# Kernel optimization log

Measured on AMD Instinct MI355X. Metric: run time of the kernel, lower is better.

## Reference

```python
import jax, jax.numpy as jnp
import numpy as np

H = 8           # num_heads
TANH_CLIP = 10.0


def setup_inputs() -> dict:
    key = jax.random.key(0)
    ks = jax.random.split(key, 7)
    B, N, D = 512, 1000, 128
    embeddings = jax.random.normal(ks[0], (B, N, D), dtype=jnp.float32)
    context_feat = jax.random.normal(ks[1], (B, 2 * D), dtype=jnp.float32)
    W_node = jax.random.normal(ks[2], (D, 3 * D), dtype=jnp.float32) / np.sqrt(D)
    W_fixed = jax.random.normal(ks[3], (D, D), dtype=jnp.float32) / np.sqrt(D)
    W_step = jax.random.normal(ks[4], (2 * D, D), dtype=jnp.float32) / np.sqrt(2 * D)
    W_out = jax.random.normal(ks[5], (D, D), dtype=jnp.float32) / np.sqrt(D)
    # action_mask: True = feasible node; ensure at least one feasible per row
    action_mask = jax.random.uniform(ks[6], (B, N)) > 0.3
    action_mask = action_mask.at[:, 0].set(True)
    return {"embeddings": embeddings, "context_feat": context_feat,
            "W_node": W_node, "W_fixed": W_fixed, "W_step": W_step,
            "W_out": W_out, "action_mask": action_mask}


def reference(embeddings, context_feat, W_node, W_fixed, W_step, W_out, action_mask):
    B, N, D = embeddings.shape
    dk = D // H
    # --- _precompute ---
    graph_context = (embeddings.mean(axis=1) @ W_fixed)[:, None, :]      # [B,1,D]
    proj = embeddings @ W_node                                            # [B,N,3D]
    gk, gv, logit_k = jnp.split(proj, 3, axis=-1)                         # each [B,N,D]
    to_heads = lambda x: x.reshape(B, N, H, dk).transpose(2, 0, 1, 3)     # [H,B,N,dk]
    K, V = to_heads(gk), to_heads(gv)
    # --- _get_log_p: query (num_steps = 1) ---
    q = graph_context + (context_feat @ W_step)[:, None, :]               # [B,1,D]
    Q = q.reshape(B, 1, H, dk).transpose(2, 0, 1, 3)                      # [H,B,1,dk]
    mask = ~action_mask                                                    # [B,N], True = infeasible
    # --- glimpse attention (mask_inner) ---
    compat = jnp.einsum('hbqd,hbnd->hbqn', Q, K) / jnp.sqrt(jnp.asarray(dk, Q.dtype))
    compat = jnp.where(mask[None, :, None, :], -jnp.inf, compat)
    attn = jax.nn.softmax(compat, axis=-1)                                 # [H,B,1,N]
    heads = jnp.einsum('hbqn,hbnd->hbqd', attn, V)                         # [H,B,1,dk]
    glimpse = heads.transpose(1, 2, 0, 3).reshape(B, 1, D) @ W_out         # [B,1,D]
    # --- tanh-clipped single-head logits ---
    logits = jnp.einsum('bqd,bnd->bqn', glimpse, logit_k) / jnp.sqrt(jnp.asarray(D, glimpse.dtype))
    logits = jnp.tanh(logits) * TANH_CLIP
    logits = jnp.where(mask[:, None, :], -jnp.inf, logits)                 # [B,1,N]
    return logits
```

## Files before the change

kernel.cpp:

```cpp
#include <hip/hip_runtime.h>
#include <math.h>

#define BB 512
#define NN 1000
#define DD 128
#define HH 8
#define TILE 64
#define NT 16

#define WS_AFOLD 4096

__device__ __forceinline__ bool mask_feasible(const void* mask, int flag, int idx) {
    if (flag == 1) return ((const int*)mask)[idx] != 0;
    if (flag == 2) return ((const float*)mask)[idx] != 0.0f;
    return ((const unsigned char*)mask)[idx] != 0;
}

__device__ __forceinline__ void gload_lds16(const float4* g, float4* l) {
    __builtin_amdgcn_global_load_lds(
        (const __attribute__((address_space(1))) void*)g,
        (__attribute__((address_space(3))) void*)l,
        16, 0, 0);
}

__global__ void k0_detect(const unsigned int* __restrict__ m, int* __restrict__ flag) {
    int t = threadIdx.x;
    unsigned int w = m[t];
    unsigned long long bi = __ballot(w <= 1u);
    unsigned long long bf = __ballot(w == 0u || w == 0x3F800000u);
    if (t == 0) {
        int f = 0;
        if (bi == ~0ull) f = 1;
        else if (bf == ~0ull) f = 2;
        *flag = f;
    }
}

__global__ __launch_bounds__(512) void kA_meanfold(
    const float* __restrict__ emb, const float* __restrict__ ctx,
    const float* __restrict__ W_fixed, const float* __restrict__ W_step,
    const float* __restrict__ W_node, float* __restrict__ Afold) {
    int b = blockIdx.x, t = threadIdx.x;
    __shared__ float4 red[512];
    __shared__ float mean_s[DD], cld[2 * DD], qlds[DD];
    int q4 = t & 31, j = t >> 5;
    const float4* e4 = (const float4*)(emb + (size_t)b * NN * DD);
    float4 acc = {0.f, 0.f, 0.f, 0.f};
    for (int n = j; n < NN; n += 16) {
        float4 v = e4[n * 32 + q4];
        acc.x += v.x; acc.y += v.y; acc.z += v.z; acc.w += v.w;
    }
    red[t] = acc;
    __syncthreads();
    for (int s = 8; s >= 1; s >>= 1) {
        if (j < s) {
            float4 o = red[t + s * 32], m = red[t];
            m.x += o.x; m.y += o.y; m.z += o.z; m.w += o.w;
            red[t] = m;
        }
        __syncthreads();
    }
    if (t < 32) {
        float4 m = red[t];
        const float inv = 1.0f / (float)NN;
        ((float4*)mean_s)[t] = make_float4(m.x * inv, m.y * inv, m.z * inv, m.w * inv);
    }
    if (t < 256) cld[t] = ctx[b * 2 * DD + t];
    __syncthreads();
    if (t < 128) {
        float a = 0.f;
        for (int c = 0; c < DD; ++c)     a += mean_s[c] * W_fixed[c * DD + t];
        for (int c = 0; c < 2 * DD; ++c) a += cld[c] * W_step[c * DD + t];
        qlds[t] = a;
    }
    __syncthreads();
    if (t < 128) {
        const float* wrow = W_node + (size_t)t * 3 * DD;
        float* A2 = Afold + (size_t)b * 1024;
        for (int h = 0; h < HH; ++h) {
            float a = 0.f;
#pragma unroll
            for (int d0 = 0; d0 < 16; ++d0) a += wrow[h * 16 + d0] * qlds[h * 16 + d0];
            A2[t * 8 + h] = 0.25f * a;
        }
    }
}

__global__ __launch_bounds__(256) void kB_flash(
    const float* __restrict__ emb, const float* __restrict__ Afold,
    const void* __restrict__ mask, const int* __restrict__ flagp,
    const float* __restrict__ W_node, const float* __restrict__ W_out,
    float* __restrict__ out) {
    int b = blockIdx.x, t = threadIdx.x;
    int flag = *flagp;
    int wave = t >> 6, lane = t & 63;
    int hq = wave * 2;
    int n = lane;
    int c4 = t & 31, jr = t >> 5;

    __shared__ float4 buf2[2][TILE * 32];
    __shared__ float cbufs[TILE * 8];
    __shared__ float zl[HH];

    int hqs = __builtin_amdgcn_readfirstlane(hq);
    const float* AbW = Afold + (size_t)b * 1024 + hqs;

    float4 wacc[8];
#pragma unroll
    for (int h = 0; h < HH; ++h) wacc[h] = make_float4(0.f, 0.f, 0.f, 0.f);
    float zrun = 0.f;

    const float4* embB4 = (const float4*)(emb + (size_t)b * NN * DD);
    const int mbase = b * NN;

    auto stage = [&](int dst, int n0, int rows) {
        int nchunks = (rows * 32) >> 6;
        float4* base = buf2[dst];
        for (int i = wave; i < nchunks; i += 4) {
            int p0 = i * 64;
            int p = p0 + lane;
            int r = p >> 5;
            int c = (p & 31) ^ (r & 31);
            gload_lds16(embB4 + (size_t)(n0 + r) * 32 + c, base + p0);
        }
    };

    stage(0, 0, TILE);
    __syncthreads();
    int cur = 0;

    for (int tile = 0; tile < NT; ++tile) {
        int n0 = tile * TILE;
        int rows = (NN - n0 < TILE) ? (NN - n0) : TILE;
        if (tile < NT - 1) {
            int n1 = n0 + TILE;
            int rows1 = (NN - n1 < TILE) ? (NN - n1) : TILE;
            stage(cur ^ 1, n1, rows1);
        }
        const float4* tb = buf2[cur];
        if (n < rows) {
            int sw = n & 31;
            float sx = 0.f, sy = 0.f;
#pragma unroll 8
            for (int k = 0; k < 32; ++k) {
                float4 e = tb[n * 32 + (k ^ sw)];
                const float* ak = AbW + k * 32;
                sx += e.x * ak[0] + e.y * ak[8] + e.z * ak[16] + e.w * ak[24];
                sy += e.x * ak[1] + e.y * ak[9] + e.z * ak[17] + e.w * ak[25];
            }
            bool feas = mask_feasible(mask, flag, mbase + n0 + n);
            cbufs[n * 8 + hq]     = feas ? __expf(sx) : 0.f;
            cbufs[n * 8 + hq + 1] = feas ? __expf(sy) : 0.f;
        }
        __syncthreads();
        if (t < 64) {
            int h = t & 7, seg = t >> 3;
            float z = 0.f;
            for (int nn = seg; nn < rows; nn += 8) z += cbufs[nn * 8 + h];
            z += __shfl_xor(z, 8);
            z += __shfl_xor(z, 16);
            z += __shfl_xor(z, 32);
            if (t < 8) zrun += z;
        }
        for (int nn = jr; nn < rows; nn += 8) {
            float4 e = tb[nn * 32 + (c4 ^ (nn & 31))];
            float4 pA = *(const float4*)&cbufs[nn * 8];
            float4 pB = *(const float4*)&cbufs[nn * 8 + 4];
            wacc[0].x += pA.x * e.x; wacc[0].y += pA.x * e.y; wacc[0].z += pA.x * e.z; wacc[0].w += pA.x * e.w;
            wacc[1].x += pA.y * e.x; wacc[1].y += pA.y * e.y; wacc[1].z += pA.y * e.z; wacc[1].w += pA.y * e.w;
            wacc[2].x += pA.z * e.x; wacc[2].y += pA.z * e.y; wacc[2].z += pA.z * e.z; wacc[2].w += pA.z * e.w;
            wacc[3].x += pA.w * e.x; wacc[3].y += pA.w * e.y; wacc[3].z += pA.w * e.z; wacc[3].w += pA.w * e.w;
            wacc[4].x += pB.x * e.x; wacc[4].y += pB.x * e.y; wacc[4].z += pB.x * e.z; wacc[4].w += pB.x * e.w;
            wacc[5].x += pB.y * e.x; wacc[5].y += pB.y * e.y; wacc[5].z += pB.y * e.z; wacc[5].w += pB.y * e.w;
            wacc[6].x += pB.z * e.x; wacc[6].y += pB.z * e.y; wacc[6].z += pB.z * e.z; wacc[6].w += pB.z * e.w;
            wacc[7].x += pB.w * e.x; wacc[7].y += pB.w * e.y; wacc[7].z += pB.w * e.z; wacc[7].w += pB.w * e.w;
        }
        __syncthreads();
        cur ^= 1;
    }
    if (t < 8) zl[t] = zrun;
    float4 wsum;
    {
        float4* red = (float4*)buf2;
#pragma unroll
        for (int h = 0; h < HH; ++h) red[(jr * 32 + c4) * 8 + h] = wacc[h];
        __syncthreads();
        int cc = t >> 3, hh = t & 7;
        float4 s = make_float4(0.f, 0.f, 0.f, 0.f);
#pragma unroll
        for (int jj = 0; jj < 8; ++jj) {
            float4 v = red[(jj * 32 + cc) * 8 + hh];
            s.x += v.x; s.y += v.y; s.z += v.z; s.w += v.w;
        }
        float inv = 1.0f / zl[hh];
        wsum = make_float4(s.x * inv, s.y * inv, s.z * inv, s.w * inv);
    }
    __syncthreads();
    float* wemb_s = (float*)buf2;
    float* small  = (float*)buf2 + 1024;
    {
        int cc = t >> 3, hh = t & 7;
        *(float4*)&wemb_s[hh * 128 + cc * 4] = wsum;
    }
    __syncthreads();
    if (t < 128) {
        int h = t >> 4;
        float a = 0.f;
        for (int c = 0; c < DD; ++c) a += wemb_s[h * 128 + c] * W_node[(size_t)c * 384 + 128 + t];
        small[t] = a;
    }
    __syncthreads();
    if (t < 128) {
        float g = 0.f;
        for (int k = 0; k < DD; ++k) g += small[k] * W_out[k * DD + t];
        small[128 + t] = g;
    }
    __syncthreads();
    if (t < 128) {
        float a3 = 0.f;
        const float* wr = W_node + (size_t)t * 384 + 256;
        for (int d = 0; d < DD; ++d) a3 += wr[d] * small[128 + d];
        small[256 + t] = a3;
    }
    __syncthreads();
    const float4* g2v = (const float4*)&small[256];
    for (int r = t; r < NN; r += 256) {
        const float4* row = embB4 + (size_t)r * 32;
        float acc = 0.f;
#pragma unroll 8
        for (int k = 0; k < 32; ++k) {
            float4 e = row[k], g = g2v[k];
            acc += e.x * g.x + e.y * g.y + e.z * g.z + e.w * g.w;
        }
        bool feas = mask_feasible(mask, flag, mbase + r);
        out[(size_t)mbase + r] = feas ? (10.0f * tanhf(acc * 0.08838834764831845f)) : -1.0e30f;
    }
}

extern "C" void kernel_launch(void* const* d_in, const int* in_sizes, int n_in,
                              void* d_out, int out_size, void* d_ws, size_t ws_size,
                              hipStream_t stream) {
    (void)in_sizes; (void)n_in; (void)out_size; (void)ws_size;
    const float* emb     = (const float*)d_in[0];
    const float* ctx     = (const float*)d_in[1];
    const float* W_node  = (const float*)d_in[2];
    const float* W_fixed = (const float*)d_in[3];
    const float* W_step  = (const float*)d_in[4];
    const float* W_out   = (const float*)d_in[5];
    const void*  mask    = d_in[6];
    float* out = (float*)d_out;

    char* ws = (char*)d_ws;
    int*   flag  = (int*)(ws + 0);
    float* Afold = (float*)(ws + WS_AFOLD);

    k0_detect<<<1, 64, 0, stream>>>((const unsigned int*)mask, flag);
    kA_meanfold<<<BB, 512, 0, stream>>>(emb, ctx, W_fixed, W_step, W_node, Afold);
    kB_flash<<<BB, 256, 0, stream>>>(emb, Afold, mask, flag, W_node, W_out, out);
}
```

Baseline: 185.2 us.

## Fuse mask-type detection into meanfold, preload mask to LDS, relax tile barrier

Moves the mask dtype detection into the first block of the mean/fold kernel, which removes one kernel launch. The flash kernel now loads the per-row mask into shared memory once as floats and multiplies by it instead of branching on global mask reads inside the tile loop and the output loop. The per-tile __syncthreads is replaced with an LDS-only wait plus a raw s_barrier, so outstanding global-to-LDS prefetches are not drained before the barrier. The LDS footprint grows (mfl, and separate wemb_s/small arrays), which may reduce occupancy, and the relaxed barrier relies on the prefetched buffer being waited on somewhere later.

```diff
diff --git a/kernel.cpp b/kernel.cpp
--- a/kernel.cpp
+++ b/kernel.cpp
@@ -23,24 +23,23 @@
         16, 0, 0);
 }
 
-__global__ void k0_detect(const unsigned int* __restrict__ m, int* __restrict__ flag) {
-    int t = threadIdx.x;
-    unsigned int w = m[t];
-    unsigned long long bi = __ballot(w <= 1u);
-    unsigned long long bf = __ballot(w == 0u || w == 0x3F800000u);
-    if (t == 0) {
-        int f = 0;
-        if (bi == ~0ull) f = 1;
-        else if (bf == ~0ull) f = 2;
-        *flag = f;
-    }
-}
-
 __global__ __launch_bounds__(512) void kA_meanfold(
     const float* __restrict__ emb, const float* __restrict__ ctx,
     const float* __restrict__ W_fixed, const float* __restrict__ W_step,
-    const float* __restrict__ W_node, float* __restrict__ Afold) {
+    const float* __restrict__ W_node, float* __restrict__ Afold,
+    const unsigned int* __restrict__ maskw, int* __restrict__ flag) {
     int b = blockIdx.x, t = threadIdx.x;
+    if (b == 0 && t < 64) {
+        unsigned int w = maskw[t];
+        unsigned long long bi = __ballot(w <= 1u);
+        unsigned long long bf = __ballot(w == 0u || w == 0x3F800000u);
+        if (t == 0) {
+            int f = 0;
+            if (bi == ~0ull) f = 1;
+            else if (bf == ~0ull) f = 2;
+            *flag = f;
+        }
+    }
     __shared__ float4 red[512];
     __shared__ float mean_s[DD], cld[2 * DD], qlds[DD];
     int q4 = t & 31, j = t >> 5;
@@ -65,7 +64,7 @@
         const float inv = 1.0f / (float)NN;
         ((float4*)mean_s)[t] = make_float4(m.x * inv, m.y * inv, m.z * inv, m.w * inv);
     }
-    if (t < 256) cld[t] = ctx[b * 2 * DD + t];
+    if (t >= 256) cld[t - 256] = ctx[b * 2 * DD + (t - 256)];
     __syncthreads();
     if (t < 128) {
         float a = 0.f;
@@ -95,11 +94,13 @@
     int flag = *flagp;
     int wave = t >> 6, lane = t & 63;
     int hq = wave * 2;
-    int n = lane;
     int c4 = t & 31, jr = t >> 5;
 
     __shared__ float4 buf2[2][TILE * 32];
     __shared__ float cbufs[TILE * 8];
+    __shared__ float mfl[NN];
+    __shared__ float wemb_s[8][128];
+    __shared__ float small[3 * DD];
     __shared__ float zl[HH];
 
     int hqs = __builtin_amdgcn_readfirstlane(hq);
@@ -125,6 +126,8 @@
         }
     };
 
+    for (int r = t; r < NN; r += 256)
+        mfl[r] = mask_feasible(mask, flag, mbase + r) ? 1.0f : 0.0f;
     stage(0, 0, TILE);
     __syncthreads();
     int cur = 0;
@@ -138,8 +141,8 @@
             stage(cur ^ 1, n1, rows1);
         }
         const float4* tb = buf2[cur];
-        if (n < rows) {
-            int sw = n & 31;
+        if (lane < rows) {
+            int n = lane, sw = lane & 31;
             float sx = 0.f, sy = 0.f;
 #pragma unroll 8
             for (int k = 0; k < 32; ++k) {
@@ -148,11 +151,14 @@
                 sx += e.x * ak[0] + e.y * ak[8] + e.z * ak[16] + e.w * ak[24];
                 sy += e.x * ak[1] + e.y * ak[9] + e.z * ak[17] + e.w * ak[25];
             }
-            bool feas = mask_feasible(mask, flag, mbase + n0 + n);
-            cbufs[n * 8 + hq]     = feas ? __expf(sx) : 0.f;
-            cbufs[n * 8 + hq + 1] = feas ? __expf(sy) : 0.f;
-        }
-        __syncthreads();
+            float fm = mfl[n0 + n];
+            cbufs[n * 8 + hq]     = fm * __expf(sx);
+            cbufs[n * 8 + hq + 1] = fm * __expf(sy);
+        }
+        asm volatile("s_waitcnt lgkmcnt(0)" ::: "memory");
+        __builtin_amdgcn_sched_barrier(0);
+        __builtin_amdgcn_s_barrier();
+        __builtin_amdgcn_sched_barrier(0);
         if (t < 64) {
             int h = t & 7, seg = t >> 3;
             float z = 0.f;
@@ -196,17 +202,15 @@
         wsum = make_float4(s.x * inv, s.y * inv, s.z * inv, s.w * inv);
     }
     __syncthreads();
-    float* wemb_s = (float*)buf2;
-    float* small  = (float*)buf2 + 1024;
     {
         int cc = t >> 3, hh = t & 7;
-        *(float4*)&wemb_s[hh * 128 + cc * 4] = wsum;
+        *(float4*)&wemb_s[hh][cc * 4] = wsum;
     }
     __syncthreads();
     if (t < 128) {
         int h = t >> 4;
         float a = 0.f;
-        for (int c = 0; c < DD; ++c) a += wemb_s[h * 128 + c] * W_node[(size_t)c * 384 + 128 + t];
+        for (int c = 0; c < DD; ++c) a += wemb_s[h][c] * W_node[(size_t)c * 384 + 128 + t];
         small[t] = a;
     }
     __syncthreads();
@@ -232,8 +236,8 @@
             float4 e = row[k], g = g2v[k];
             acc += e.x * g.x + e.y * g.y + e.z * g.z + e.w * g.w;
         }
-        bool feas = mask_feasible(mask, flag, mbase + r);
-        out[(size_t)mbase + r] = feas ? (10.0f * tanhf(acc * 0.08838834764831845f)) : -1.0e30f;
+        out[(size_t)mbase + r] = (mfl[r] != 0.0f)
+            ? (10.0f * tanhf(acc * 0.08838834764831845f)) : -1.0e30f;
     }
 }
 
@@ -254,7 +258,7 @@
     int*   flag  = (int*)(ws + 0);
     float* Afold = (float*)(ws + WS_AFOLD);
 
-    k0_detect<<<1, 64, 0, stream>>>((const unsigned int*)mask, flag);
-    kA_meanfold<<<BB, 512, 0, stream>>>(emb, ctx, W_fixed, W_step, W_node, Afold);
+    kA_meanfold<<<BB, 512, 0, stream>>>(emb, ctx, W_fixed, W_step, W_node, Afold,
+                                        (const unsigned int*)mask, flag);
     kB_flash<<<BB, 256, 0, stream>>>(emb, Afold, mask, flag, W_node, W_out, out);
 }
```

New measurement: 176.0 us. -4.9%, faster.
